# Kernel tuning notes

Hardware: AMD Instinct MI355X
Metric: run time of the kernel (lower is better)

## Reference

```python
import jax, jax.numpy as jnp
import numpy as np

N = 10000   # nodes
E = 100000  # edges (before self-loops)
H = 4       # heads (layers 0-3); last layer uses 1 head
C = 200     # out_channels per head
IN_DIMS = [200, H * C, H * C, H * C, H * C]
HEADS   = [H, H, H, H, 1]
NEG_SLOPE = 0.2  # PyG GATConv default


def _gat_layer(x, src, dst, W, a_src, a_dst, b, heads):
    # x: [N, Fin], W: [Fin, heads*C], a_src/a_dst: [heads, C], b: [heads*C]
    h = (x @ W).reshape(N, heads, C)                       # [N,H,C]
    alpha_src = jnp.einsum('nhc,hc->nh', h, a_src)         # [N,H]
    alpha_dst = jnp.einsum('nhc,hc->nh', h, a_dst)         # [N,H]
    e = jax.nn.leaky_relu(alpha_src[src] + alpha_dst[dst], NEG_SLOPE)  # [E',H]
    # segment softmax over incoming edges of each dst node
    m = jax.ops.segment_max(e, dst, num_segments=N)        # [N,H]
    ex = jnp.exp(e - m[dst])                               # [E',H]
    den = jax.ops.segment_sum(ex, dst, num_segments=N)     # [N,H]
    alpha = ex / den[dst]                                  # [E',H]
    out = jax.ops.segment_sum(h[src] * alpha[:, :, None], dst, num_segments=N)
    return out.reshape(N, heads * C) + b, alpha


def setup_inputs() -> dict:
    key = jax.random.key(0)
    ks = jax.random.split(key, 2 + 4 * 5)
    inp = {}
    inp['X'] = jax.random.normal(ks[0], (N, 200), jnp.float32)
    inp['edge_index'] = jax.random.randint(ks[1], (2, E), 0, N, dtype=jnp.int32)
    k = 2
    for i in range(5):
        fin, hd = IN_DIMS[i], HEADS[i]
        s = 1.0 / np.sqrt(fin)
        inp[f'W{i}'] = jax.random.normal(ks[k], (fin, hd * C), jnp.float32) * s; k += 1
        inp[f'as{i}'] = jax.random.normal(ks[k], (hd, C), jnp.float32) * s; k += 1
        inp[f'ad{i}'] = jax.random.normal(ks[k], (hd, C), jnp.float32) * s; k += 1
        inp[f'b{i}'] = jnp.zeros((hd * C,), jnp.float32); k += 1
    return inp


def reference(X, edge_index,
              W0, as0, ad0, b0, W1, as1, ad1, b1, W2, as2, ad2, b2,
              W3, as3, ad3, b3, W4, as4, ad4, b4):
    # add self-loops (PyG GATConv default add_self_loops=True)
    loops = jnp.arange(N, dtype=edge_index.dtype)
    src = jnp.concatenate([edge_index[0], loops])
    dst = jnp.concatenate([edge_index[1], loops])
    gelu = lambda v: jax.nn.gelu(v, approximate=False)
    # eval mode: all dropouts are identity
    x, _ = _gat_layer(X, src, dst, W0, as0, ad0, b0, HEADS[0]); x = gelu(x)
    x, _ = _gat_layer(x, src, dst, W1, as1, ad1, b1, HEADS[1]); x = gelu(x)
    x, _ = _gat_layer(x, src, dst, W2, as2, ad2, b2, HEADS[2]); x = gelu(x)
    x, _ = _gat_layer(x, src, dst, W3, as3, ad3, b3, HEADS[3]); x = gelu(x)
    x, edge_attn = _gat_layer(x, src, dst, W4, as4, ad4, b4, HEADS[4])
    x = gelu(x)
    return (x, edge_attn)
```

## Files before the change

kernel.cpp:

```cpp
#include <hip/hip_runtime.h>
#include <math.h>

#define NN 10000
#define EE 100000
#define EPE 110000
#define CC 200
#define MPAD 10112

typedef __attribute__((ext_vector_type(8))) _Float16 f16x8;
typedef __attribute__((ext_vector_type(4))) _Float16 f16x4;
typedef __attribute__((ext_vector_type(4))) unsigned short u16x4;
typedef __attribute__((ext_vector_type(4))) float f32x4;

__device__ __forceinline__ float lrelu(float v) { return v >= 0.f ? v : 0.2f * v; }
__device__ __forceinline__ float gelu_f(float v) { return 0.5f * v * (1.f + erff(v * 0.70710678118654752f)); }


__global__ void build_edges_kernel(const int* __restrict__ ei,
                                   int* __restrict__ src_all, int* __restrict__ dst_all,
                                   int* __restrict__ deg) {
    int e = blockIdx.x * blockDim.x + threadIdx.x;
    if (e >= EPE) return;
    int s, d;
    if (e < EE) { s = ei[e]; d = ei[EE + e]; }
    else        { s = e - EE; d = e - EE; }
    src_all[e] = s;
    dst_all[e] = d;
    atomicAdd(&deg[d], 1);
}

__global__ void scan_kernel(const int* __restrict__ deg, int* __restrict__ row_ptr, int n) {
    __shared__ int wsum[16];
    int tid = threadIdx.x;
    int lane = tid & 63, w = tid >> 6;
    int carry = 0;
    for (int base = 0; base < n; base += 1024) {
        int idx = base + tid;
        int v = (idx < n) ? deg[idx] : 0;
        int x = v;
#pragma unroll
        for (int off = 1; off < 64; off <<= 1) {
            int t = __shfl_up(x, off);
            if (lane >= off) x += t;
        }
        if (lane == 63) wsum[w] = x;
        __syncthreads();
        if (w == 0) {
            int s = (lane < 16) ? wsum[lane] : 0;
#pragma unroll
            for (int off = 1; off < 16; off <<= 1) {
                int t = __shfl_up(s, off);
                if (lane >= off) s += t;
            }
            if (lane < 16) wsum[lane] = s;
        }
        __syncthreads();
        int woff = (w > 0) ? wsum[w - 1] : 0;
        if (idx < n) row_ptr[idx] = carry + woff + x - v;
        carry += wsum[15];
        __syncthreads();
    }
    if (tid == 0) row_ptr[n] = carry;
}

__global__ void scatter_kernel(const int* __restrict__ src_all, const int* __restrict__ dst_all,
                               const int* __restrict__ row_ptr, int* __restrict__ cursor,
                               int* __restrict__ col_src, int* __restrict__ col_eid) {
    int e = blockIdx.x * blockDim.x + threadIdx.x;
    if (e >= EPE) return;
    int d = dst_all[e];
    int pos = row_ptr[d] + atomicAdd(&cursor[d], 1);
    col_src[pos] = src_all[e];
    col_eid[pos] = e;
}


__global__ void convA_kernel(const float* __restrict__ x, int sx, int Fin, int Kp,
                             unsigned short* __restrict__ Ap) {
    size_t idx = (size_t)blockIdx.x * 256 + threadIdx.x;
    if (idx >= (size_t)MPAD * Kp) return;
    int row = (int)(idx / Kp);
    int kk  = (int)(idx % Kp);
    float v = 0.f;
    if (row < NN && kk < Fin) v = x[(size_t)row * sx + kk];
    Ap[idx] = __builtin_bit_cast(unsigned short, (_Float16)v);
}

__global__ void padA_kernel(unsigned short* __restrict__ Ap) {
    int idx = blockIdx.x * 256 + threadIdx.x;
    if (idx < NN * 32) {
        int rw = idx >> 5, c = idx & 31;
        Ap[(size_t)rw * 832 + 800 + c] = 0;
    } else {
        int j = idx - NN * 32;
        if (j < (MPAD - NN) * 832) {
            int rw = j / 832, c = j - rw * 832;
            Ap[(size_t)(NN + rw) * 832 + c] = 0;
        }
    }
}

__global__ void convB_all_kernel(const float* __restrict__ W0, const float* __restrict__ W1,
                                 const float* __restrict__ W2, const float* __restrict__ W3,
                                 const float* __restrict__ W4,
                                 unsigned short* __restrict__ Bp) {
    int l = blockIdx.y;
    const float* W = (l == 0) ? W0 : (l == 1) ? W1 : (l == 2) ? W2 : (l == 3) ? W3 : W4;
    int Fin = (l == 0) ? 200 : 800;
    int HC  = (l == 4) ? 200 : 800;
    int Kp  = (l == 0) ? 256 : 832;
    int Np  = (l == 4) ? 256 : 896;
    int idx = blockIdx.x * 256 + threadIdx.x;
    if (idx >= Np * Kp) return;
    int n = idx / Kp, kk = idx - n * Kp;
    float v = 0.f;
    if (n < HC && kk < Fin) v = W[(size_t)kk * HC + n];
    Bp[(size_t)l * (896 * 832) + idx] = __builtin_bit_cast(unsigned short, (_Float16)v);
}


__global__ __launch_bounds__(256) void gemm_mfma(const unsigned short* __restrict__ A,
                                                 const unsigned short* __restrict__ B,
                                                 unsigned short* __restrict__ C,
                                                 const float* __restrict__ a_s,
                                                 const float* __restrict__ a_d,
                                                 float* __restrict__ g_as,
                                                 float* __restrict__ g_ad,
                                                 int Kt, int Np, int ncol, int HC, int H) {
    __shared__ unsigned short As[2][4096];
    __shared__ unsigned short Bs[2][8192];

    int tid = threadIdx.x;
    int lane = tid & 63, wave = tid >> 6;

    int nwg = gridDim.x;
    int orig = blockIdx.x;
    int q = nwg >> 3, r = nwg & 7;
    int xcd = orig & 7, sidx = orig >> 3;
    int wg = (xcd < r ? xcd * (q + 1) : r * (q + 1) + (xcd - r) * q) + sidx;
    int rowT = wg / ncol, colT = wg - rowT * ncol;
    int row0 = rowT * 64, col0 = colT * 128;
    int wr = wave >> 1, wc = wave & 1;

    size_t gAoff[2], gBoff[4];
    int ldsSegA[2], ldsSegB[4];
#pragma unroll
    for (int i = 0; i < 2; ++i) {
        int seg = wave * 2 + i;
        int chunkIdx = seg * 64 + lane;
        int rr = chunkIdx >> 3;
        int c = chunkIdx & 7;
        int cg = c ^ (rr & 7);
        gAoff[i] = (size_t)(row0 + rr) * Kt + (size_t)cg * 8;
        ldsSegA[i] = seg * 512;
    }
#pragma unroll
    for (int i = 0; i < 4; ++i) {
        int seg = wave * 4 + i;
        int chunkIdx = seg * 64 + lane;
        int rr = chunkIdx >> 3;
        int c = chunkIdx & 7;
        int cg = c ^ (rr & 7);
        gBoff[i] = (size_t)(col0 + rr) * Kt + (size_t)cg * 8;
        ldsSegB[i] = seg * 512;
    }

    int rowA[2], rowB[4];
#pragma unroll
    for (int m = 0; m < 2; ++m) rowA[m] = wr * 32 + m * 16 + (lane & 15);
#pragma unroll
    for (int n = 0; n < 4; ++n) rowB[n] = wc * 64 + n * 16 + (lane & 15);

    f32x4 acc[2][4];
#pragma unroll
    for (int m = 0; m < 2; ++m)
#pragma unroll
        for (int n = 0; n < 4; ++n) acc[m][n] = f32x4{0.f, 0.f, 0.f, 0.f};

#define STAGE(bufi, kk)                                                                     \
    _Pragma("unroll")                                                                       \
    for (int i = 0; i < 2; ++i)                                                             \
        __builtin_amdgcn_global_load_lds(                                                   \
            (const __attribute__((address_space(1))) void*)(A + gAoff[i] + (kk)),           \
            (__attribute__((address_space(3))) void*)(&As[bufi][ldsSegA[i]]), 16, 0, 0);    \
    _Pragma("unroll")                                                                       \
    for (int i = 0; i < 4; ++i)                                                             \
        __builtin_amdgcn_global_load_lds(                                                   \
            (const __attribute__((address_space(1))) void*)(B + gBoff[i] + (kk)),           \
            (__attribute__((address_space(3))) void*)(&Bs[bufi][ldsSegB[i]]), 16, 0, 0);

    int nk = Kt >> 6;
    STAGE(0, 0)

    for (int t = 0; t < nk; ++t) {
        int cur = t & 1;
        if (t + 1 < nk) {
            STAGE(1 - cur, (t + 1) * 64)
            asm volatile("s_waitcnt vmcnt(6)" ::: "memory");
        } else {
            asm volatile("s_waitcnt vmcnt(0)" ::: "memory");
        }
        __builtin_amdgcn_s_barrier();
        __builtin_amdgcn_sched_barrier(0);

        const unsigned short* asb = As[cur];
        const unsigned short* bsb = Bs[cur];
#pragma unroll
        for (int kh = 0; kh < 2; ++kh) {
            int cw = kh * 4 + (lane >> 4);
            f16x8 a[2], b[4];
#pragma unroll
            for (int m = 0; m < 2; ++m) {
                int ia = rowA[m] * 64 + ((cw ^ (rowA[m] & 7)) << 3);
                a[m] = *(const f16x8*)(&asb[ia]);
            }
#pragma unroll
            for (int n = 0; n < 4; ++n) {
                int ib = rowB[n] * 64 + ((cw ^ (rowB[n] & 7)) << 3);
                b[n] = *(const f16x8*)(&bsb[ib]);
            }
            if (kh == 0) __builtin_amdgcn_s_setprio(1);
#pragma unroll
            for (int m = 0; m < 2; ++m)
#pragma unroll
                for (int n = 0; n < 4; ++n)
                    acc[m][n] = __builtin_amdgcn_mfma_f32_16x16x32_f16(a[m], b[n], acc[m][n], 0, 0, 0);
        }
        __builtin_amdgcn_s_setprio(0);
        asm volatile("s_waitcnt lgkmcnt(0)" ::: "memory");
        __builtin_amdgcn_sched_barrier(0);
        __builtin_amdgcn_s_barrier();
        __builtin_amdgcn_sched_barrier(0);
    }
#undef STAGE

    int crow = row0 + wr * 32 + ((lane >> 4) << 2);
    int ccol = col0 + wc * 64 + (lane & 15);
#pragma unroll
    for (int m = 0; m < 2; ++m)
#pragma unroll
        for (int j = 0; j < 4; ++j) {
            size_t rb = (size_t)(crow + m * 16 + j) * Np;
#pragma unroll
            for (int n = 0; n < 4; ++n)
                C[rb + ccol + n * 16] =
                    __builtin_bit_cast(unsigned short, (_Float16)acc[m][n][j]);
        }

    int base = col0 + wc * 64;
    int hA = base / CC;
    float sAs[2][8], sAd[2][8];
#pragma unroll
    for (int b = 0; b < 2; ++b)
#pragma unroll
        for (int k = 0; k < 8; ++k) { sAs[b][k] = 0.f; sAd[b][k] = 0.f; }
#pragma unroll
    for (int n = 0; n < 4; ++n) {
        int c = ccol + n * 16;
        if (c < HC) {
            int hd = c / CC;
            int cm = c - hd * CC;
            float asv = a_s[hd * CC + cm];
            float adv = a_d[hd * CC + cm];
            int b = hd - hA;
#pragma unroll
            for (int m = 0; m < 2; ++m)
#pragma unroll
                for (int j = 0; j < 4; ++j) {
                    sAs[b][m * 4 + j] += acc[m][n][j] * asv;
                    sAd[b][m * 4 + j] += acc[m][n][j] * adv;
                }
        }
    }
#pragma unroll
    for (int off = 1; off < 16; off <<= 1) {
#pragma unroll
        for (int b = 0; b < 2; ++b)
#pragma unroll
            for (int k = 0; k < 8; ++k) {
                sAs[b][k] += __shfl_xor(sAs[b][k], off);
                sAd[b][k] += __shfl_xor(sAd[b][k], off);
            }
    }
    if ((lane & 15) == 0) {
        int slice = colT * 2 + wc;
        float* pas = g_as + (size_t)slice * NN * H;
        float* pad2 = g_ad + (size_t)slice * NN * H;
#pragma unroll
        for (int b = 0; b < 2; ++b) {
            int hd = hA + b;
            if (hd >= H) continue;
#pragma unroll
            for (int m = 0; m < 2; ++m)
#pragma unroll
                for (int j = 0; j < 4; ++j) {
                    int row = crow + m * 16 + j;
                    if (row < NN) {
                        pas[row * H + hd] = sAs[b][m * 4 + j];
                        pad2[row * H + hd] = sAd[b][m * 4 + j];
                    }
                }
        }
    }
}

__global__ void fold_attn_kernel(const float* __restrict__ g_as, const float* __restrict__ g_ad,
                                 float* __restrict__ asrc, float* __restrict__ adst, int H) {
    int i = blockIdx.x * 256 + threadIdx.x;
    if (i >= NN * H) return;
    int hd = i % H;
    int w0 = (CC * hd) >> 6, w1 = (CC * hd + CC - 1) >> 6;
    float sa = 0.f, sd = 0.f;
    for (int w = w0; w <= w1; ++w) {
        sa += g_as[(size_t)w * NN * H + i];
        sd += g_ad[(size_t)w * NN * H + i];
    }
    asrc[i] = sa;
    adst[i] = sd;
}


__global__ __launch_bounds__(256) void fused_agg_kernel(const unsigned short* __restrict__ h,
                                                        const float* __restrict__ asrc,
                                                        const float* __restrict__ adst,
                                                        const int* __restrict__ row_ptr,
                                                        const int* __restrict__ col_src,
                                                        const int* __restrict__ col_eid,
                                                        const float* __restrict__ bias,
                                                        float* __restrict__ out32,
                                                        unsigned short* __restrict__ apn,
                                                        float* __restrict__ wout,
                                                        int H, int HC, int HCp) {
    int n = blockIdx.x;
    int tid = threadIdx.x;
    int wave = tid >> 6, lane = tid & 63;
    int beg = row_ptr[n], end = row_ptr[n + 1];

    __shared__ float m_s[4], inv_s[4], ad_s[4];
    __shared__ float w_lds[64 * 4];
    __shared__ int src_lds[64];

    if (wave < H) {
        float ad = adst[n * H + wave];
        float m = -1e30f, den = 0.f;
        for (int e = beg + lane; e < end; e += 64) {
            float v = lrelu(asrc[col_src[e] * H + wave] + ad);
            if (v > m) { den = den * expf(m - v) + 1.f; m = v; }
            else den += expf(v - m);
        }
#pragma unroll
        for (int off = 1; off < 64; off <<= 1) {
            float m2 = __shfl_xor(m, off);
            float d2 = __shfl_xor(den, off);
            float M = fmaxf(m, m2);
            den = den * expf(m - M) + d2 * expf(m2 - M);
            m = M;
        }
        if (lane == 0) { m_s[wave] = m; inv_s[wave] = 1.f / den; ad_s[wave] = ad; }
    }
    __syncthreads();

    int ch0 = tid * 4;
    int head = ch0 / CC;
    float a0 = 0.f, a1 = 0.f, a2 = 0.f, a3 = 0.f;

    for (int c0 = beg; c0 < end; c0 += 64) {
        int cnt = min(64, end - c0);
        if (wave < H && lane < cnt) {
            int e = c0 + lane;
            int s = col_src[e];
            float v = lrelu(asrc[s * H + wave] + ad_s[wave]);
            float wv = expf(v - m_s[wave]) * inv_s[wave];
            w_lds[lane * 4 + wave] = wv;
            if (wave == 0) src_lds[lane] = s;
            if (wout) wout[(size_t)col_eid[e] * H + wave] = wv;
        }
        __syncthreads();
        if (ch0 < HC) {
            int s = src_lds[0];
            float wv = w_lds[head];
            f16x4 hv = *(const f16x4*)(h + (size_t)s * HCp + ch0);
            for (int j = 0; j < cnt; ++j) {
                float wv2 = 0.f; f16x4 hv2 = {};
                if (j + 1 < cnt) {
                    int s2 = src_lds[j + 1];
                    wv2 = w_lds[(j + 1) * 4 + head];
                    hv2 = *(const f16x4*)(h + (size_t)s2 * HCp + ch0);
                }
                a0 += wv * (float)hv[0];
                a1 += wv * (float)hv[1];
                a2 += wv * (float)hv[2];
                a3 += wv * (float)hv[3];
                wv = wv2; hv = hv2;
            }
        }
        __syncthreads();
    }

    if (ch0 < HC) {
        float4 bv = *(const float4*)(bias + ch0);
        float g0 = gelu_f(a0 + bv.x), g1 = gelu_f(a1 + bv.y);
        float g2 = gelu_f(a2 + bv.z), g3 = gelu_f(a3 + bv.w);
        if (out32) {
            *(float4*)(out32 + (size_t)n * HC + ch0) = float4{g0, g1, g2, g3};
        } else {
            *(u16x4*)(apn + (size_t)n * 832 + ch0) = u16x4{
                __builtin_bit_cast(unsigned short, (_Float16)g0),
                __builtin_bit_cast(unsigned short, (_Float16)g1),
                __builtin_bit_cast(unsigned short, (_Float16)g2),
                __builtin_bit_cast(unsigned short, (_Float16)g3)};
        }
    }
}


extern "C" void kernel_launch(void* const* d_in, const int* in_sizes, int n_in,
                              void* d_out, int out_size, void* d_ws, size_t ws_size,
                              hipStream_t stream) {
    const float* X = (const float*)d_in[0];
    const int* ei = (const int*)d_in[1];

    char* ws = (char*)d_ws;
    size_t off = 0;
    auto alloc = [&](size_t bytes) { void* p = ws + off; off += (bytes + 255) & ~(size_t)255; return p; };

    unsigned short* Ap0 = (unsigned short*)alloc((size_t)MPAD * 256 * 2);
    unsigned short* Ap  = (unsigned short*)alloc((size_t)MPAD * 832 * 2);
    unsigned short* Bp  = (unsigned short*)alloc((size_t)5 * 896 * 832 * 2);
    unsigned short* hbuf= (unsigned short*)alloc((size_t)MPAD * 896 * 2);
    float* g_as  = (float*)alloc((size_t)14 * NN * 4 * 4);
    float* g_ad  = (float*)alloc((size_t)14 * NN * 4 * 4);
    float* attn_all = (float*)alloc((size_t)5 * 2 * NN * 4 * 4);
    int* src_all  = (int*)alloc((size_t)EPE * 4);
    int* dst_all  = (int*)alloc((size_t)EPE * 4);
    int* col_src  = (int*)alloc((size_t)EPE * 4);
    int* col_eid  = (int*)alloc((size_t)EPE * 4);
    int* row_ptr  = (int*)alloc((size_t)(NN + 1) * 4);
    int* degcur   = (int*)alloc((size_t)2 * NN * 4);
    int* deg = degcur, * cursor = degcur + NN;

    hipMemsetAsync(degcur, 0, 2 * NN * sizeof(int), stream);

    int eb = (EPE + 255) / 256;
    build_edges_kernel<<<eb, 256, 0, stream>>>(ei, src_all, dst_all, deg);
    scan_kernel<<<1, 1024, 0, stream>>>(deg, row_ptr, NN);
    scatter_kernel<<<eb, 256, 0, stream>>>(src_all, dst_all, row_ptr, cursor, col_src, col_eid);

    {
        int npad = NN * 32 + (MPAD - NN) * 832;
        padA_kernel<<<(npad + 255) / 256, 256, 0, stream>>>(Ap);
    }
    {
        size_t na = (size_t)MPAD * 256;
        convA_kernel<<<(int)((na + 255) / 256), 256, 0, stream>>>(X, 200, 200, 256, Ap0);
    }
    convB_all_kernel<<<dim3((896 * 832 + 255) / 256, 5), 256, 0, stream>>>(
        (const float*)d_in[2], (const float*)d_in[6], (const float*)d_in[10],
        (const float*)d_in[14], (const float*)d_in[18], Bp);

    for (int i = 0; i < 5; ++i) {
        int H   = (i == 4) ? 1 : 4;
        int HC  = H * CC;
        int Kp  = (i == 0) ? 256 : 832;
        int Np  = (i == 4) ? 256 : 896;
        int ncol = Np / 128;
        const unsigned short* Acur = (i == 0) ? Ap0 : Ap;
        const unsigned short* Bpl = Bp + (size_t)i * (896 * 832);
        const float* as_ = (const float*)d_in[3 + 4 * i];
        const float* ad_ = (const float*)d_in[4 + 4 * i];
        const float* b_  = (const float*)d_in[5 + 4 * i];
        float* asrc_l = attn_all + (size_t)i * 2 * NN * 4;
        float* adst_l = asrc_l + NN * 4;

        gemm_mfma<<<ncol * (MPAD / 64), 256, 0, stream>>>(Acur, Bpl, hbuf, as_, ad_,
                                                          g_as, g_ad, Kp, Np, ncol, HC, H);

        fold_attn_kernel<<<(NN * H + 255) / 256, 256, 0, stream>>>(g_as, g_ad,
                                                                   asrc_l, adst_l, H);

        float* out32 = (i == 4) ? (float*)d_out : nullptr;
        unsigned short* apn = (i == 4) ? nullptr : Ap;
        float* wout = (i == 4) ? (float*)d_out + (size_t)NN * CC : nullptr;
        fused_agg_kernel<<<NN, 256, 0, stream>>>(hbuf, asrc_l, adst_l, row_ptr, col_src,
                                                 col_eid, b_, out32, apn, wout, H, HC, Np);
    }
}
```

Baseline: 549.2 us.

## Triple-buffer GEMM LDS pipeline and deepen gather prefetch in aggregation

Moves the MFMA GEMM from double to triple buffering in LDS, issuing global-to-LDS loads two k-tiles ahead and adjusting vmcnt waits to match. The swizzled LDS read offsets are now computed once outside the k-loop. The aggregation kernel's neighbour-feature gather now prefetches two rows ahead instead of one, to hide more gather latency. The cost is 50% more LDS per block, which may lower occupancy, plus extra registers for the offsets and prefetch buffers.

```diff
diff --git a/kernel.cpp b/kernel.cpp
--- a/kernel.cpp
+++ b/kernel.cpp
@@ -127,8 +127,8 @@
                                                  float* __restrict__ g_as,
                                                  float* __restrict__ g_ad,
                                                  int Kt, int Np, int ncol, int HC, int H) {
-    __shared__ unsigned short As[2][4096];
-    __shared__ unsigned short Bs[2][8192];
+    __shared__ unsigned short As[3][4096];
+    __shared__ unsigned short Bs[3][8192];
 
     int tid = threadIdx.x;
     int lane = tid & 63, wave = tid >> 6;
@@ -170,6 +170,18 @@
     for (int m = 0; m < 2; ++m) rowA[m] = wr * 32 + m * 16 + (lane & 15);
 #pragma unroll
     for (int n = 0; n < 4; ++n) rowB[n] = wc * 64 + n * 16 + (lane & 15);
+
+    int iaOff[2][2], ibOff[2][4];
+#pragma unroll
+    for (int kh = 0; kh < 2; ++kh) {
+        int cw = kh * 4 + (lane >> 4);
+#pragma unroll
+        for (int m = 0; m < 2; ++m)
+            iaOff[kh][m] = rowA[m] * 64 + ((cw ^ (rowA[m] & 7)) << 3);
+#pragma unroll
+        for (int n = 0; n < 4; ++n)
+            ibOff[kh][n] = rowB[n] * 64 + ((cw ^ (rowB[n] & 7)) << 3);
+    }
 
     f32x4 acc[2][4];
 #pragma unroll
@@ -191,15 +203,18 @@
 
     int nk = Kt >> 6;
     STAGE(0, 0)
-
+    if (nk > 1) STAGE(1, 64)
+
+    int cur = 0;
     for (int t = 0; t < nk; ++t) {
-        int cur = t & 1;
-        if (t + 1 < nk) {
-            STAGE(1 - cur, (t + 1) * 64)
-            asm volatile("s_waitcnt vmcnt(6)" ::: "memory");
-        } else {
-            asm volatile("s_waitcnt vmcnt(0)" ::: "memory");
-        }
+        if (t + 2 < nk) {
+            int b2 = cur + 2; if (b2 >= 3) b2 -= 3;
+            STAGE(b2, (t + 2) * 64)
+        }
+        int rem = nk - 1 - t;
+        if (rem >= 2)      { asm volatile("s_waitcnt vmcnt(12)" ::: "memory"); }
+        else if (rem == 1) { asm volatile("s_waitcnt vmcnt(6)"  ::: "memory"); }
+        else               { asm volatile("s_waitcnt vmcnt(0)"  ::: "memory"); }
         __builtin_amdgcn_s_barrier();
         __builtin_amdgcn_sched_barrier(0);
 
@@ -207,18 +222,11 @@
         const unsigned short* bsb = Bs[cur];
 #pragma unroll
         for (int kh = 0; kh < 2; ++kh) {
-            int cw = kh * 4 + (lane >> 4);
             f16x8 a[2], b[4];
 #pragma unroll
-            for (int m = 0; m < 2; ++m) {
-                int ia = rowA[m] * 64 + ((cw ^ (rowA[m] & 7)) << 3);
-                a[m] = *(const f16x8*)(&asb[ia]);
-            }
-#pragma unroll
-            for (int n = 0; n < 4; ++n) {
-                int ib = rowB[n] * 64 + ((cw ^ (rowB[n] & 7)) << 3);
-                b[n] = *(const f16x8*)(&bsb[ib]);
-            }
+            for (int m = 0; m < 2; ++m) a[m] = *(const f16x8*)(&asb[iaOff[kh][m]]);
+#pragma unroll
+            for (int n = 0; n < 4; ++n) b[n] = *(const f16x8*)(&bsb[ibOff[kh][n]]);
             if (kh == 0) __builtin_amdgcn_s_setprio(1);
 #pragma unroll
             for (int m = 0; m < 2; ++m)
@@ -231,6 +239,7 @@
         __builtin_amdgcn_sched_barrier(0);
         __builtin_amdgcn_s_barrier();
         __builtin_amdgcn_sched_barrier(0);
+        cur = (cur + 1 == 3) ? 0 : cur + 1;
     }
 #undef STAGE
 
@@ -377,21 +386,18 @@
         }
         __syncthreads();
         if (ch0 < HC) {
-            int s = src_lds[0];
-            float wv = w_lds[head];
-            f16x4 hv = *(const f16x4*)(h + (size_t)s * HCp + ch0);
+            f16x4 hva = {}, hvb = {};
+            hva = *(const f16x4*)(h + (size_t)src_lds[0] * HCp + ch0);
+            if (cnt > 1) hvb = *(const f16x4*)(h + (size_t)src_lds[1] * HCp + ch0);
             for (int j = 0; j < cnt; ++j) {
-                float wv2 = 0.f; f16x4 hv2 = {};
-                if (j + 1 < cnt) {
-                    int s2 = src_lds[j + 1];
-                    wv2 = w_lds[(j + 1) * 4 + head];
-                    hv2 = *(const f16x4*)(h + (size_t)s2 * HCp + ch0);
-                }
-                a0 += wv * (float)hv[0];
-                a1 += wv * (float)hv[1];
-                a2 += wv * (float)hv[2];
-                a3 += wv * (float)hv[3];
-                wv = wv2; hv = hv2;
+                f16x4 hvc = {};
+                if (j + 2 < cnt) hvc = *(const f16x4*)(h + (size_t)src_lds[j + 2] * HCp + ch0);
+                float wv = w_lds[j * 4 + head];
+                a0 += wv * (float)hva[0];
+                a1 += wv * (float)hva[1];
+                a2 += wv * (float)hva[2];
+                a3 += wv * (float)hva[3];
+                hva = hvb; hvb = hvc;
             }
         }
         __syncthreads();
```

After: 571.7 us. 4.1% more time.
